# Kernel tuning notes

Hardware: AMD Instinct MI355X
Metric: run time of the kernel (lower is better)

Reference implementation:

```python
import jax, jax.numpy as jnp
import numpy as np

INPUT_DIM = 512
HIDDEN_DIM = 256
REP_DIM = 256
SCORE_HIDDEN = 128


def setup_inputs() -> dict:
    key = jax.random.key(0)
    ks = jax.random.split(key, 12)
    def rn(k, shape, scale=None):
        s = scale if scale is not None else 1.0 / np.sqrt(shape[0])
        return jax.random.normal(k, shape, dtype=jnp.float32) * s
    return {
        "feat_x": jax.random.normal(ks[0], (512, INPUT_DIM), dtype=jnp.float32),
        "feat_pos": jax.random.normal(ks[1], (512, INPUT_DIM), dtype=jnp.float32),
        "feat_neg": jax.random.normal(ks[2], (512, INPUT_DIM), dtype=jnp.float32),
        # g: Linear(input,hidden) -> GELU -> Linear(hidden,rep); stored as x @ W
        "g_w1": rn(ks[3], (INPUT_DIM, HIDDEN_DIM)),
        "g_b1": jnp.zeros((HIDDEN_DIM,), jnp.float32),
        "g_w2": rn(ks[4], (HIDDEN_DIM, REP_DIM)),
        "g_b2": jnp.zeros((REP_DIM,), jnp.float32),
        # out_proj: Linear(rep, input, bias=False)
        "out_w": rn(ks[5], (REP_DIM, INPUT_DIM)),
        # score_net: Linear(3*rep+1, score_hidden) -> GELU -> Linear(score_hidden, 1)
        "s_w1": rn(ks[6], (3 * REP_DIM + 1, SCORE_HIDDEN)),
        "s_b1": jnp.zeros((SCORE_HIDDEN,), jnp.float32),
        "s_w2": rn(ks[7], (SCORE_HIDDEN, 1)),
        "s_b2": jnp.zeros((1,), jnp.float32),
    }


def _gelu(x):
    return jax.nn.gelu(x, approximate=False)  # torch nn.GELU default = exact erf


def _g(x, g_w1, g_b1, g_w2, g_b2):
    return _gelu(x @ g_w1 + g_b1) @ g_w2 + g_b2


def _set_operator(feat_x, feat_set, params):
    g_w1, g_b1, g_w2, g_b2, out_w, s_w1, s_b1, s_w2, s_b2 = params
    x_rep = _g(feat_x, g_w1, g_b1, g_w2, g_b2)   # (n, r)
    y_rep = _g(feat_set, g_w1, g_b1, g_w2, g_b2)  # (m, r)
    n, r = x_rep.shape
    m = y_rep.shape[0]
    x_exp = jnp.broadcast_to(x_rep[:, None, :], (n, m, r))
    y_exp = jnp.broadcast_to(y_rep[None, :, :], (n, m, r))
    delta = y_exp - x_exp                                   # (n, m, r)
    delta_norm = jnp.linalg.norm(delta, axis=-1, keepdims=True)
    score_in = jnp.concatenate([x_exp, y_exp, delta, delta_norm], axis=-1)  # (n, m, 3r+1)
    logits = (_gelu(score_in @ s_w1 + s_b1) @ s_w2 + s_b2)[..., 0]          # (n, m)
    weights = jax.nn.softmax(logits, axis=1)
    set_update_rep = jnp.einsum("nm,nmr->nr", weights, delta)
    return set_update_rep @ out_w


def reference(feat_x, feat_pos, feat_neg, g_w1, g_b1, g_w2, g_b2, out_w, s_w1, s_b1, s_w2, s_b2):
    params = (g_w1, g_b1, g_w2, g_b2, out_w, s_w1, s_b1, s_w2, s_b2)
    s_pos = _set_operator(feat_x, feat_pos, params)
    s_neg = _set_operator(feat_x, feat_neg, params)  # mask_self_neg=False
    return s_pos - s_neg
```

## Files before the change

kernel.cpp:

```cpp
#include <hip/hip_runtime.h>
#include <math.h>

#define NN 512
#define IN 512
#define HD 256
#define RD 256
#define SH 128

__device__ __forceinline__ float gelu_fast(float x){
    const float z  = x * 0.70710678118654752f;
    const float az = fabsf(z);
    const float t  = __builtin_amdgcn_rcpf(fmaf(0.3275911f, az, 1.0f));
    float p = fmaf(1.061405429f, t, -1.453152027f);
    p = fmaf(p, t, 1.421413741f);
    p = fmaf(p, t, -0.284496736f);
    p = fmaf(p, t, 0.254829592f);
    p = p * t;
    const float e = __builtin_amdgcn_exp2f(z * z * -1.4426950408889634f);
    const float E = p * e;
    const float one_plus_erf = (x >= 0.0f) ? (2.0f - E) : E;
    return 0.5f * x * one_plus_erf;
}

__device__ __forceinline__ float gelu2(float u){
    const float az = fabsf(u);
    const float tt = __builtin_amdgcn_rcpf(fmaf(0.23166045f, az, 1.0f));
    float p = fmaf(1.061405429f, tt, -1.453152027f);
    p = fmaf(p, tt, 1.421413741f);
    p = fmaf(p, tt, -0.284496736f);
    p = fmaf(p, tt, 0.254829592f);
    p = p * tt;
    const float e2 = __builtin_amdgcn_exp2f(u * u * -0.72134752044448170f);
    const float Eq = p * e2;
    const float ope = (u >= 0.0f) ? (2.0f - Eq) : Eq;
    return u * ope;
}

__global__ __launch_bounds__(512) void k_rep(
    const float* __restrict__ fx, const float* __restrict__ fp, const float* __restrict__ fn,
    const float* __restrict__ w1, const float* __restrict__ b1,
    const float* __restrict__ w2, const float* __restrict__ b2,
    const float* __restrict__ s_w1,
    float* __restrict__ r_x, float* __restrict__ r_p, float* __restrict__ r_n,
    float* __restrict__ rT_p, float* __restrict__ rT_n,
    float* __restrict__ A_x, float* __restrict__ BT_p, float* __restrict__ BT_n)
{
    __shared__ float xs[4][IN];
    __shared__ float ps[8][4][HD];
    __shared__ float hs[4][HD];
    __shared__ float rloc[4][RD];
    __shared__ float ab4[4][SH];
    const int t = threadIdx.x;
    const int mat = blockIdx.x >> 7;
    const int row0 = (blockIdx.x & 127) << 2;
    const float* src = (mat==0) ? fx : (mat==1) ? fp : fn;

    {
        const int j = t >> 7, c4 = (t & 127) << 2;
        *(float4*)&xs[j][c4] = *(const float4*)&src[(row0+j)*IN + c4];
    }
    __syncthreads();

    const int cg = t & 63, s = t >> 6;
    const int c0 = cg << 2;

    {
        float4 acc[4];
        #pragma unroll
        for (int j=0;j<4;j++) acc[j] = make_float4(0.f,0.f,0.f,0.f);
        const float* wp = w1 + (s*64)*HD + c0;
        #pragma unroll 8
        for (int ii=0; ii<64; ii++){
            float4 w = *(const float4*)wp; wp += HD;
            const int i = s*64 + ii;
            #pragma unroll
            for (int j=0;j<4;j++){
                const float xv = xs[j][i];
                acc[j].x = fmaf(xv, w.x, acc[j].x);
                acc[j].y = fmaf(xv, w.y, acc[j].y);
                acc[j].z = fmaf(xv, w.z, acc[j].z);
                acc[j].w = fmaf(xv, w.w, acc[j].w);
            }
        }
        #pragma unroll
        for (int j=0;j<4;j++) *(float4*)&ps[s][j][c0] = acc[j];
    }
    __syncthreads();

    #pragma unroll
    for (int rep=0; rep<2; rep++){
        const int idx = rep*512 + t;
        const int j = idx >> 8, c = idx & 255;
        float v = b1[c];
        #pragma unroll
        for (int ss=0; ss<8; ss++) v += ps[ss][j][c];
        hs[j][c] = gelu_fast(v);
    }
    __syncthreads();

    {
        float4 acc[4];
        #pragma unroll
        for (int j=0;j<4;j++) acc[j] = make_float4(0.f,0.f,0.f,0.f);
        const float* wp = w2 + (s*32)*RD + c0;
        #pragma unroll 8
        for (int ii=0; ii<32; ii++){
            float4 w = *(const float4*)wp; wp += RD;
            const int i = s*32 + ii;
            #pragma unroll
            for (int j=0;j<4;j++){
                const float xv = hs[j][i];
                acc[j].x = fmaf(xv, w.x, acc[j].x);
                acc[j].y = fmaf(xv, w.y, acc[j].y);
                acc[j].z = fmaf(xv, w.z, acc[j].z);
                acc[j].w = fmaf(xv, w.w, acc[j].w);
            }
        }
        #pragma unroll
        for (int j=0;j<4;j++) *(float4*)&ps[s][j][c0] = acc[j];
    }
    __syncthreads();

    float* rout = (mat==0) ? r_x : (mat==1) ? r_p : r_n;
    #pragma unroll
    for (int rep=0; rep<2; rep++){
        const int idx = rep*512 + t;
        const int j = idx >> 8, c = idx & 255;
        float v = b2[c];
        #pragma unroll
        for (int ss=0; ss<8; ss++) v += ps[ss][j][c];
        rloc[j][c] = v;
        rout[(row0+j)*RD + c] = v;
    }
    __syncthreads();

    if (mat && t < 256){
        float* rT = (mat==1) ? rT_p : rT_n;
        float4 q = make_float4(rloc[0][t], rloc[1][t], rloc[2][t], rloc[3][t]);
        *(float4*)&rT[t*NN + row0] = q;
    }

    {
        const int cg2 = t & 31, s2 = t >> 5;
        const int cc0 = cg2 << 2;
        const float sgn = (mat==0) ? -1.0f : 1.0f;
        const int base1 = (mat==0) ? 0 : 256;
        const float* p1 = s_w1 + (base1 + s2*16)*SH + cc0;
        const float* p3 = s_w1 + (512   + s2*16)*SH + cc0;
        float4 a[4];
        #pragma unroll
        for (int j=0;j<4;j++) a[j] = make_float4(0.f,0.f,0.f,0.f);
        #pragma unroll 8
        for (int ii=0; ii<16; ii++){
            float4 wa = *(const float4*)p1; p1 += SH;
            float4 wd = *(const float4*)p3; p3 += SH;
            float4 w;
            w.x = fmaf(sgn, wd.x, wa.x);
            w.y = fmaf(sgn, wd.y, wa.y);
            w.z = fmaf(sgn, wd.z, wa.z);
            w.w = fmaf(sgn, wd.w, wa.w);
            const int i = s2*16 + ii;
            #pragma unroll
            for (int j=0;j<4;j++){
                const float xv = rloc[j][i];
                a[j].x = fmaf(xv, w.x, a[j].x);
                a[j].y = fmaf(xv, w.y, a[j].y);
                a[j].z = fmaf(xv, w.z, a[j].z);
                a[j].w = fmaf(xv, w.w, a[j].w);
            }
        }
        float* psf = &ps[0][0][0];
        #pragma unroll
        for (int j=0;j<4;j++) *(float4*)&psf[(s2*4 + j)*SH + cc0] = a[j];
    }
    __syncthreads();

    {
        const float* psf = &ps[0][0][0];
        const int j = t >> 7, c = t & 127;
        float v = 0.f;
        #pragma unroll
        for (int ss=0; ss<16; ss++) v += psf[(ss*4 + j)*SH + c];
        if (mat==0) A_x[(row0+j)*SH + c] = v;
        else        ab4[j][c] = v;
    }
    __syncthreads();
    if (mat && t < 128){
        float* BT = (mat==1) ? BT_p : BT_n;
        float4 q = make_float4(ab4[0][t], ab4[1][t], ab4[2][t], ab4[3][t]);
        *(float4*)&BT[t*NN + row0] = q;
    }
}

__global__ __launch_bounds__(256) void k_sd(
    const float* __restrict__ r_x, const float* __restrict__ rT_p, const float* __restrict__ rT_n,
    const float* __restrict__ A_x, const float* __restrict__ BT_p, const float* __restrict__ BT_n,
    const float* __restrict__ r_p, const float* __restrict__ r_n,
    const float* __restrict__ s_w1, const float* __restrict__ s_b1,
    const float* __restrict__ s_w2,
    float* __restrict__ psum, float* __restrict__ Spart)
{
    __shared__ float2 xs2[RD];
    __shared__ float4 cmb[SH];
    __shared__ float pda[2][128];
    __shared__ float pdb[2][128];
    __shared__ float pdc[2][128];
    __shared__ float2 evb[128];
    __shared__ float nx[2];
    __shared__ float ssum[2][2];
    const int t = threadIdx.x;
    const int set = blockIdx.x >> 10;
    const int rem = blockIdx.x & 1023;
    const int n0 = (rem >> 2) << 1;
    const int mt = rem & 3;
    const int mbase = mt << 7;
    const int tm = t & 127, kh = t >> 7;
    const int m = mbase + tm;
    const float* yT = set ? rT_n : rT_p;
    const float* BT = set ? BT_n : BT_p;

    xs2[t] = make_float2(r_x[n0*RD + t], r_x[(n0+1)*RD + t]);
    if (t < SH){
        const float b1v = s_b1[t];
        cmb[t] = make_float4(A_x[n0*SH + t] + b1v,
                             A_x[(n0+1)*SH + t] + b1v,
                             s_w1[768*SH + t],
                             0.5f * s_w2[t]);
    }
    __syncthreads();

    if (t < 128){
        const int w = t >> 6, l = t & 63;
        float v = 0.f;
        #pragma unroll
        for (int q=0;q<4;q++){
            const float2 e = xs2[l + 64*q];
            const float ev = w ? e.y : e.x;
            v = fmaf(ev, ev, v);
        }
        #pragma unroll
        for (int off=32; off>=1; off>>=1) v += __shfl_xor(v, off);
        if (l==0) nx[w] = v;
    }

    float d0=0.f, d1=0.f, ny=0.f;
    {
        const float* yp = yT + (kh << 7)*NN + m;
        #pragma unroll 16
        for (int rr=0; rr<128; rr++){
            const float y = yp[rr*NN];
            const float2 xv = xs2[(kh << 7) + rr];
            d0 = fmaf(xv.x, y, d0);
            d1 = fmaf(xv.y, y, d1);
            ny = fmaf(y, y, ny);
        }
    }
    pda[kh][tm] = d0; pdb[kh][tm] = d1; pdc[kh][tm] = ny;
    __syncthreads();
    d0 += pda[1-kh][tm]; d1 += pdb[1-kh][tm]; ny += pdc[1-kh][tm];
    const float dn0 = sqrtf(fmaxf(fmaf(-2.f, d0, nx[0] + ny), 0.f));
    const float dn1 = sqrtf(fmaxf(fmaf(-2.f, d1, nx[1] + ny), 0.f));

    float acc0 = 0.f, acc1 = 0.f;
    {
        const float* bp = BT + (kh << 6)*NN + m;
        #pragma unroll 4
        for (int kk=0; kk<64; kk++){
            const float b = bp[kk*NN];
            const float4 c = cmb[(kh << 6) + kk];
            const float u0 = fmaf(dn0, c.z, c.x + b);
            const float u1 = fmaf(dn1, c.z, c.y + b);
            acc0 = fmaf(c.w, gelu2(u0), acc0);
            acc1 = fmaf(c.w, gelu2(u1), acc1);
        }
    }
    __syncthreads();
    pda[kh][tm] = acc0; pdb[kh][tm] = acc1;
    __syncthreads();
    if (kh == 0){
        const float ev0 = __builtin_amdgcn_exp2f((acc0 + pda[1][tm]) * 1.4426950408889634f);
        const float ev1 = __builtin_amdgcn_exp2f((acc1 + pdb[1][tm]) * 1.4426950408889634f);
        evb[tm] = make_float2(ev0, ev1);
        float v0 = ev0, v1 = ev1;
        #pragma unroll
        for (int off=32; off>=1; off>>=1){ v0 += __shfl_xor(v0, off); v1 += __shfl_xor(v1, off); }
        if ((t & 63) == 0){
            ssum[tm >> 6][0] = v0;
            ssum[tm >> 6][1] = v1;
        }
    }
    __syncthreads();
    if (t < 2)
        Spart[(set*4 + mt)*NN + n0 + t] = ssum[0][t] + ssum[1][t];

    {
        const float* ry = (set ? r_n : r_p) + mbase*RD + t;
        float a0 = 0.f, a1 = 0.f;
        #pragma unroll 8
        for (int mm=0; mm<128; mm++){
            const float rv = ry[mm*RD];
            const float2 w = evb[mm];
            a0 = fmaf(w.x, rv, a0);
            a1 = fmaf(w.y, rv, a1);
        }
        float* P = psum + ((set*4 + mt)*NN + n0)*RD;
        P[t]      = a0;
        P[RD + t] = a1;
    }
}

__global__ __launch_bounds__(512) void k_fin(
    const float* __restrict__ psum, const float* __restrict__ Spart,
    const float* __restrict__ out_w, float* __restrict__ out)
{
    __shared__ float dv[2][RD];
    const int t = threadIdx.x;
    const int np = blockIdx.x >> 1, ch = blockIdx.x & 1;
    const int n0 = np << 1;

    {
        const int j = t >> 8, c = t & 255;
        const int n = n0 + j;
        float Sp = 0.f, Sn = 0.f;
        #pragma unroll
        for (int q=0;q<4;q++){
            Sp += Spart[q*NN + n];
            Sn += Spart[(4+q)*NN + n];
        }
        float vp = 0.f, vn = 0.f;
        #pragma unroll
        for (int q=0;q<4;q++){
            vp += psum[(q*NN + n)*RD + c];
            vn += psum[((4+q)*NN + n)*RD + c];
        }
        dv[j][c] = vp * (1.0f/Sp) - vn * (1.0f/Sn);
    }
    __syncthreads();

    {
        const int j = t >> 8, col = (ch << 8) + (t & 255);
        float o = 0.f;
        const float* wo = out_w + col;
        #pragma unroll 8
        for (int r=0; r<RD; r++){ o = fmaf(dv[j][r], *wo, o); wo += IN; }
        out[(n0+j)*IN + col] = o;
    }
}

extern "C" void kernel_launch(void* const* d_in, const int* in_sizes, int n_in,
                              void* d_out, int out_size, void* d_ws, size_t ws_size,
                              hipStream_t stream)
{
    const float* fx  = (const float*)d_in[0];
    const float* fp  = (const float*)d_in[1];
    const float* fn  = (const float*)d_in[2];
    const float* gw1 = (const float*)d_in[3];
    const float* gb1 = (const float*)d_in[4];
    const float* gw2 = (const float*)d_in[5];
    const float* gb2 = (const float*)d_in[6];
    const float* ow  = (const float*)d_in[7];
    const float* sw1 = (const float*)d_in[8];
    const float* sb1 = (const float*)d_in[9];
    const float* sw2 = (const float*)d_in[10];
    float* out = (float*)d_out;

    float* ws   = (float*)d_ws;
    float* r_x  = ws;
    float* r_p  = r_x  + 131072;
    float* r_n  = r_p  + 131072;
    float* rT_p = r_n  + 131072;
    float* rT_n = rT_p + 131072;
    float* A_x  = rT_n + 131072;
    float* BT_p = A_x  + 65536;
    float* BT_n = BT_p + 65536;
    float* Spar = BT_n + 65536;
    float* psum = Spar + 4096;

    hipLaunchKernelGGL(k_rep, dim3(384), dim3(512), 0, stream,
                       fx, fp, fn, gw1, gb1, gw2, gb2, sw1,
                       r_x, r_p, r_n, rT_p, rT_n, A_x, BT_p, BT_n);
    hipLaunchKernelGGL(k_sd, dim3(2048), dim3(256), 0, stream,
                       r_x, rT_p, rT_n, A_x, BT_p, BT_n, r_p, r_n,
                       sw1, sb1, sw2, psum, Spar);
    hipLaunchKernelGGL(k_fin, dim3(512), dim3(512), 0, stream,
                       psum, Spar, ow, out);
}
```

Baseline: 159.3 us.

## Fuse final projection into score kernel via atomic ticket, precompute row norms

Removes the separate k_fin launch. The last of the 8 blocks contributing to each row pair, found through an atomic counter, performs the normalisation and out_w projection itself. Squared norms of the representations are computed once in k_rep and read in k_sd, replacing the per-block x-norm reduction and the per-thread y*y accumulation. The erf polynomial in gelu2 is also swapped for a cheaper 3-term approximation, which trades some accuracy for fewer instructions in the inner loop. The tail work now runs on only 256 threads per finishing block, and it adds a threadfence plus an atomic to every block.

```diff
diff --git a/kernel.cpp b/kernel.cpp
--- a/kernel.cpp
+++ b/kernel.cpp
@@ -24,14 +24,10 @@
 
 __device__ __forceinline__ float gelu2(float u){
     const float az = fabsf(u);
-    const float tt = __builtin_amdgcn_rcpf(fmaf(0.23166045f, az, 1.0f));
-    float p = fmaf(1.061405429f, tt, -1.453152027f);
-    p = fmaf(p, tt, 1.421413741f);
-    p = fmaf(p, tt, -0.284496736f);
-    p = fmaf(p, tt, 0.254829592f);
-    p = p * tt;
+    const float tt = __builtin_amdgcn_rcpf(fmaf(0.3326725f, az, 1.0f));
+    const float P  = fmaf(fmaf(0.7478556f, tt, -0.0958798f), tt, 0.3480242f) * tt;
     const float e2 = __builtin_amdgcn_exp2f(u * u * -0.72134752044448170f);
-    const float Eq = p * e2;
+    const float Eq = P * e2;
     const float ope = (u >= 0.0f) ? (2.0f - Eq) : Eq;
     return u * ope;
 }
@@ -43,7 +39,9 @@
     const float* __restrict__ s_w1,
     float* __restrict__ r_x, float* __restrict__ r_p, float* __restrict__ r_n,
     float* __restrict__ rT_p, float* __restrict__ rT_n,
-    float* __restrict__ A_x, float* __restrict__ BT_p, float* __restrict__ BT_n)
+    float* __restrict__ A_x, float* __restrict__ BT_p, float* __restrict__ BT_n,
+    float* __restrict__ nx2, float* __restrict__ np2, float* __restrict__ nn2,
+    int* __restrict__ cnt)
 {
     __shared__ float xs[4][IN];
     __shared__ float ps[8][4][HD];
@@ -55,6 +53,8 @@
     const int row0 = (blockIdx.x & 127) << 2;
     const float* src = (mat==0) ? fx : (mat==1) ? fp : fn;
 
+    if (blockIdx.x == 0 && t < 256) cnt[t] = 0;
+
     {
         const int j = t >> 7, c4 = (t & 127) << 2;
         *(float4*)&xs[j][c4] = *(const float4*)&src[(row0+j)*IN + c4];
@@ -134,6 +134,18 @@
     }
     __syncthreads();
 
+    if (t < 256){
+        const int w = t >> 6, l = t & 63;
+        float v = 0.f;
+        #pragma unroll
+        for (int q=0;q<4;q++){ const float e = rloc[w][l + 64*q]; v = fmaf(e,e,v); }
+        #pragma unroll
+        for (int off=32; off>=1; off>>=1) v += __shfl_xor(v, off);
+        if (l==0){
+            float* nrm = (mat==0) ? nx2 : (mat==1) ? np2 : nn2;
+            nrm[row0 + w] = v;
+        }
+    }
     if (mat && t < 256){
         float* rT = (mat==1) ? rT_p : rT_n;
         float4 q = make_float4(rloc[0][t], rloc[1][t], rloc[2][t], rloc[3][t]);
@@ -196,22 +208,26 @@
     const float* __restrict__ r_x, const float* __restrict__ rT_p, const float* __restrict__ rT_n,
     const float* __restrict__ A_x, const float* __restrict__ BT_p, const float* __restrict__ BT_n,
     const float* __restrict__ r_p, const float* __restrict__ r_n,
+    const float* __restrict__ nx2, const float* __restrict__ np2, const float* __restrict__ nn2,
     const float* __restrict__ s_w1, const float* __restrict__ s_b1,
-    const float* __restrict__ s_w2,
-    float* __restrict__ psum, float* __restrict__ Spart)
+    const float* __restrict__ s_w2, const float* __restrict__ out_w,
+    float* __restrict__ psum, float* __restrict__ Spart,
+    int* __restrict__ cnt, float* __restrict__ out)
 {
     __shared__ float2 xs2[RD];
     __shared__ float4 cmb[SH];
     __shared__ float pda[2][128];
     __shared__ float pdb[2][128];
-    __shared__ float pdc[2][128];
+    __shared__ float ny2v[128];
     __shared__ float2 evb[128];
-    __shared__ float nx[2];
     __shared__ float ssum[2][2];
+    __shared__ float dv[2][RD];
+    __shared__ int ticket;
     const int t = threadIdx.x;
     const int set = blockIdx.x >> 10;
     const int rem = blockIdx.x & 1023;
-    const int n0 = (rem >> 2) << 1;
+    const int np = rem >> 2;
+    const int n0 = np << 1;
     const int mt = rem & 3;
     const int mbase = mt << 7;
     const int tm = t & 127, kh = t >> 7;
@@ -226,24 +242,13 @@
                              A_x[(n0+1)*SH + t] + b1v,
                              s_w1[768*SH + t],
                              0.5f * s_w2[t]);
-    }
-    __syncthreads();
-
-    if (t < 128){
-        const int w = t >> 6, l = t & 63;
-        float v = 0.f;
-        #pragma unroll
-        for (int q=0;q<4;q++){
-            const float2 e = xs2[l + 64*q];
-            const float ev = w ? e.y : e.x;
-            v = fmaf(ev, ev, v);
-        }
-        #pragma unroll
-        for (int off=32; off>=1; off>>=1) v += __shfl_xor(v, off);
-        if (l==0) nx[w] = v;
-    }
-
-    float d0=0.f, d1=0.f, ny=0.f;
+        ny2v[t] = (set ? nn2 : np2)[mbase + t];
+    }
+    const float nxa = nx2[n0];
+    const float nxb = nx2[n0 + 1];
+    __syncthreads();
+
+    float d0=0.f, d1=0.f;
     {
         const float* yp = yT + (kh << 7)*NN + m;
         #pragma unroll 16
@@ -252,14 +257,14 @@
             const float2 xv = xs2[(kh << 7) + rr];
             d0 = fmaf(xv.x, y, d0);
             d1 = fmaf(xv.y, y, d1);
-            ny = fmaf(y, y, ny);
-        }
-    }
-    pda[kh][tm] = d0; pdb[kh][tm] = d1; pdc[kh][tm] = ny;
-    __syncthreads();
-    d0 += pda[1-kh][tm]; d1 += pdb[1-kh][tm]; ny += pdc[1-kh][tm];
-    const float dn0 = sqrtf(fmaxf(fmaf(-2.f, d0, nx[0] + ny), 0.f));
-    const float dn1 = sqrtf(fmaxf(fmaf(-2.f, d1, nx[1] + ny), 0.f));
+        }
+    }
+    pda[kh][tm] = d0; pdb[kh][tm] = d1;
+    __syncthreads();
+    d0 += pda[1-kh][tm]; d1 += pdb[1-kh][tm];
+    const float nyc = ny2v[tm];
+    const float dn0 = sqrtf(fmaxf(fmaf(-2.f, d0, nxa + nyc), 0.f));
+    const float dn1 = sqrtf(fmaxf(fmaf(-2.f, d1, nxb + nyc), 0.f));
 
     float acc0 = 0.f, acc1 = 0.f;
     {
@@ -307,43 +312,42 @@
         P[t]      = a0;
         P[RD + t] = a1;
     }
-}
-
-__global__ __launch_bounds__(512) void k_fin(
-    const float* __restrict__ psum, const float* __restrict__ Spart,
-    const float* __restrict__ out_w, float* __restrict__ out)
-{
-    __shared__ float dv[2][RD];
-    const int t = threadIdx.x;
-    const int np = blockIdx.x >> 1, ch = blockIdx.x & 1;
-    const int n0 = np << 1;
-
-    {
-        const int j = t >> 8, c = t & 255;
-        const int n = n0 + j;
-        float Sp = 0.f, Sn = 0.f;
-        #pragma unroll
-        for (int q=0;q<4;q++){
-            Sp += Spart[q*NN + n];
-            Sn += Spart[(4+q)*NN + n];
-        }
-        float vp = 0.f, vn = 0.f;
-        #pragma unroll
-        for (int q=0;q<4;q++){
-            vp += psum[(q*NN + n)*RD + c];
-            vn += psum[((4+q)*NN + n)*RD + c];
-        }
-        dv[j][c] = vp * (1.0f/Sp) - vn * (1.0f/Sn);
-    }
-    __syncthreads();
-
-    {
-        const int j = t >> 8, col = (ch << 8) + (t & 255);
-        float o = 0.f;
-        const float* wo = out_w + col;
-        #pragma unroll 8
-        for (int r=0; r<RD; r++){ o = fmaf(dv[j][r], *wo, o); wo += IN; }
-        out[(n0+j)*IN + col] = o;
+
+    __threadfence();
+    if (t == 0) ticket = atomicAdd(&cnt[np], 1);
+    __syncthreads();
+    if (ticket == 7){
+        __threadfence();
+        #pragma unroll
+        for (int rep=0; rep<2; rep++){
+            const int idx = rep*256 + t;
+            const int j = idx >> 8, c = idx & 255;
+            const int n = n0 + j;
+            float Sp = 0.f, Sn = 0.f;
+            #pragma unroll
+            for (int q=0;q<4;q++){
+                Sp += Spart[q*NN + n];
+                Sn += Spart[(4+q)*NN + n];
+            }
+            float vp = 0.f, vn = 0.f;
+            #pragma unroll
+            for (int q=0;q<4;q++){
+                vp += psum[(q*NN + n)*RD + c];
+                vn += psum[((4+q)*NN + n)*RD + c];
+            }
+            dv[j][c] = vp * (1.0f/Sp) - vn * (1.0f/Sn);
+        }
+        __syncthreads();
+        #pragma unroll
+        for (int q=0; q<4; q++){
+            const int j = q >> 1;
+            const int col = ((q & 1) << 8) + t;
+            float o = 0.f;
+            const float* wo = out_w + col;
+            #pragma unroll 8
+            for (int r=0; r<RD; r++){ o = fmaf(dv[j][r], *wo, o); wo += IN; }
+            out[(n0+j)*IN + col] = o;
+        }
     }
 }
 
@@ -374,14 +378,18 @@
     float* BT_p = A_x  + 65536;
     float* BT_n = BT_p + 65536;
     float* Spar = BT_n + 65536;
-    float* psum = Spar + 4096;
+    float* nx2  = Spar + 4096;
+    float* np2  = nx2  + 512;
+    float* nn2  = np2  + 512;
+    float* psum = nn2  + 512;
+    int*   cnt  = (int*)(psum + 1048576);
 
     hipLaunchKernelGGL(k_rep, dim3(384), dim3(512), 0, stream,
                        fx, fp, fn, gw1, gb1, gw2, gb2, sw1,
-                       r_x, r_p, r_n, rT_p, rT_n, A_x, BT_p, BT_n);
+                       r_x, r_p, r_n, rT_p, rT_n, A_x, BT_p, BT_n,
+                       nx2, np2, nn2, cnt);
     hipLaunchKernelGGL(k_sd, dim3(2048), dim3(256), 0, stream,
                        r_x, rT_p, rT_n, A_x, BT_p, BT_n, r_p, r_n,
-                       sw1, sb1, sw2, psum, Spar);
-    hipLaunchKernelGGL(k_fin, dim3(512), dim3(512), 0, stream,
-                       psum, Spar, ow, out);
-}
+                       nx2, np2, nn2, sw1, sb1, sw2, ow,
+                       psum, Spar, cnt, out);
+}
```

New measurement: 373.7 us. +134.5%, slower.
